# Kernel tuning notes

Measured on AMD Instinct MI355X. Metric: run time of the kernel, lower is better.

## Reference

```python
import jax, jax.numpy as jnp
import numpy as np

B, T, N = 32, 128, 30
D_T, D_V, D_I = 512, 512, 512


def setup_inputs() -> dict:
    key = jax.random.key(0)
    ks = jax.random.split(key, 9)
    return {
        "h_s": jax.random.normal(ks[0], (B, N, D_T), dtype=jnp.float32),
        "h_v": jax.random.normal(ks[1], (B, T, D_V), dtype=jnp.float32),
        "lengths": jax.random.randint(ks[2], (B,), 1, N + 1, dtype=jnp.int32),
        "W_S": jax.random.normal(ks[3], (D_T, D_I), dtype=jnp.float32) * 0.05,
        "b_S": jax.random.normal(ks[4], (D_I,), dtype=jnp.float32) * 0.05,
        "W_V": jax.random.normal(ks[5], (D_V, D_I), dtype=jnp.float32) * 0.05,
        "b_V": jax.random.normal(ks[6], (D_I,), dtype=jnp.float32) * 0.05,
        "W_w": jax.random.normal(ks[7], (D_I,), dtype=jnp.float32) * 0.05,
        "b_w": jax.random.normal(ks[8], (1,), dtype=jnp.float32) * 0.05,
    }


def reference(h_s, h_v, lengths, W_S, b_S, W_V, b_V, W_w, b_w):
    n_tok = h_s.shape[1]
    # token mask (B, N): 1 where position < length
    mask = (lengths[:, None] >= jnp.arange(1, n_tok + 1)[None, :]).astype(h_s.dtype)
    # loop-invariant projections computed once (the torch loop recomputes per t)
    S = h_s @ W_S + b_S                      # (B, N, D_I)
    V = h_v @ W_V + b_V                      # (B, T, D_I)
    # additive attention scores beta: (B, T, N)
    e = jnp.tanh(S[:, None, :, :] + V[:, :, None, :])  # (B, T, N, D_I)
    beta = jnp.einsum('btnd,d->btn', e, W_w) + b_w[0]
    # masked softmax (non-memory-efficient variant, faithful to source)
    m = mask[:, None, :]                      # (B, 1, N)
    p = jax.nn.softmax(beta * m, axis=-1) * m
    alpha = p / (p.sum(axis=-1, keepdims=True) + 1e-13) + 1e-13  # (B, T, N)
    # attended textual features: (B, T, D_T)
    return jnp.einsum('btn,bnd->btd', alpha, h_s)
```

## Files before the change

### kernel.cpp

```cpp
#include <hip/hip_runtime.h>
#include <math.h>

#define BB 32
#define TT 128
#define NTOK 30
#define DD 512
#define C2F 2.885390081777927f

typedef unsigned short u16;
typedef __attribute__((ext_vector_type(8))) short bf16x8;
typedef __attribute__((ext_vector_type(8))) unsigned short u16x8;
typedef __attribute__((ext_vector_type(4))) float f32x4;
typedef __attribute__((ext_vector_type(2))) _Float16 h16x2;

__device__ __forceinline__ u16 f2bf(float f) {
    unsigned u = __builtin_bit_cast(unsigned, f);
    u += 0x7fffu + ((u >> 16) & 1u);
    return (u16)(u >> 16);
}
__device__ __forceinline__ float bf2f(u16 u) {
    return __builtin_bit_cast(float, (unsigned)u << 16);
}
__device__ __forceinline__ u16 f2h(float f) {
    return __builtin_bit_cast(u16, (_Float16)f);
}

__device__ __forceinline__ void load_lds16(const u16* g, u16* l) {
    __builtin_amdgcn_global_load_lds(
        (const __attribute__((address_space(1))) unsigned int*)g,
        (__attribute__((address_space(3))) unsigned int*)l,
        16, 0, 0);
}

template<int CTRL>
__device__ __forceinline__ float dpp_add(float x) {
    int yi = __builtin_amdgcn_update_dpp(0, __builtin_bit_cast(int, x), CTRL, 0xF, 0xF, true);
    return x + __builtin_bit_cast(float, yi);
}
__device__ __forceinline__ float red64(float x) {
    x = dpp_add<0xB1>(x);
    x = dpp_add<0x4E>(x);
    x = dpp_add<0x141>(x);
    x = dpp_add<0x140>(x);
    x += __shfl_xor(x, 16, 64);
    x += __shfl_xor(x, 32, 64);
    return x;
}

#define NCONV ((BB*NTOK*DD + BB*TT*DD)/4/256)
__global__ __launch_bounds__(256) void prep(
    const float* __restrict__ h_s, const float* __restrict__ h_v,
    const float* __restrict__ W_S, const float* __restrict__ W_V,
    u16* __restrict__ Abf_s, u16* __restrict__ Abf_v,
    u16* __restrict__ WtS, u16* __restrict__ WtV)
{
    __shared__ u16 tile[32][33];
    int bx = blockIdx.x;
    if (bx < NCONV) {
        int i = bx * 256 + threadIdx.x;
        const int n0_4 = BB * NTOK * DD / 4;
        const float* x; u16* y;
        if (i < n0_4) { x = h_s; y = Abf_s; }
        else { i -= n0_4; x = h_v; y = Abf_v; }
        float4 v = ((const float4*)x)[i];
        ushort4 o;
        o.x = f2bf(v.x); o.y = f2bf(v.y); o.z = f2bf(v.z); o.w = f2bf(v.w);
        ((ushort4*)y)[i] = o;
        return;
    }
    int idx = bx - NCONV;
    const float* W = (idx & 256) ? W_V : W_S;
    u16*        T  = (idx & 256) ? WtV : WtS;
    idx &= 255;
    int k0 = (idx >> 4) * 32, n0 = (idx & 15) * 32;
    int c = threadIdx.x & 31, r8 = threadIdx.x >> 5;
    #pragma unroll
    for (int q = 0; q < 4; ++q) {
        int k = r8 + q * 8;
        tile[k][c] = f2bf(W[(size_t)(k0 + k) * DD + n0 + c]);
    }
    __syncthreads();
    #pragma unroll
    for (int q = 0; q < 4; ++q) {
        int n = r8 + q * 8;
        T[(size_t)(n0 + n) * DD + k0 + c] = tile[c][n];
    }
}

__global__ __launch_bounds__(256) void gemm_mfma(
    const u16* __restrict__ Abf_s, const u16* __restrict__ Abf_v,
    const u16* __restrict__ WtS, const u16* __restrict__ WtV,
    const float* __restrict__ b_S, const float* __restrict__ b_V,
    u16* __restrict__ Sh, u16* __restrict__ Vh)
{
    __shared__ u16 ldsA[64 * 64];
    __shared__ u16 ldsB[64 * 64];
    const int bid = blockIdx.x;
    const int grp = bid >> 6, rem = bid & 63;
    const int by  = rem >> 3;
    const int bxx = grp * 8 + (rem & 7);
    if (bxx >= 15 + 64) return;
    const u16* A; const u16* Bt; const float* bias; u16* Y; int bm;
    if (bxx < 15) { A = Abf_s; Bt = WtS; bias = b_S; Y = Sh; bm = bxx * 64; }
    else          { A = Abf_v; Bt = WtV; bias = b_V; Y = Vh; bm = (bxx - 15) * 64; }
    const int bn = by * 64;

    const int tid  = threadIdx.x;
    const int lane = tid & 63;
    const int wid  = tid >> 6;
    const int wr = wid >> 1, wc = wid & 1;

    const int idx0 = tid,       row0 = idx0 >> 3, ch0 = (idx0 & 7) ^ (row0 & 7);
    const int idx1 = 256 + tid, row1 = idx1 >> 3, ch1 = (idx1 & 7) ^ (row1 & 7);
    const u16* gA0 = A  + (size_t)(bm + row0) * DD + ch0 * 8;
    const u16* gA1 = A  + (size_t)(bm + row1) * DD + ch1 * 8;
    const u16* gB0 = Bt + (size_t)(bn + row0) * DD + ch0 * 8;
    const u16* gB1 = Bt + (size_t)(bn + row1) * DD + ch1 * 8;
    u16* lA0 = ldsA + wid * 512;
    u16* lA1 = ldsA + 2048 + wid * 512;
    u16* lB0 = ldsB + wid * 512;
    u16* lB1 = ldsB + 2048 + wid * 512;

    const int arow = wr * 32 + (lane & 15);
    const int brow = wc * 32 + (lane & 15);
    const int kq   = lane >> 4;
    const int sw   = lane & 7;

    f32x4 acc[2][2];
    #pragma unroll
    for (int i = 0; i < 2; ++i)
        #pragma unroll
        for (int j = 0; j < 2; ++j)
            acc[i][j] = (f32x4){0.f, 0.f, 0.f, 0.f};

    for (int k0 = 0; k0 < DD; k0 += 64) {
        __syncthreads();
        load_lds16(gA0 + k0, lA0);
        load_lds16(gA1 + k0, lA1);
        load_lds16(gB0 + k0, lB0);
        load_lds16(gB1 + k0, lB1);
        __syncthreads();

        bf16x8 af[2][2], bfr[2][2];
        #pragma unroll
        for (int i = 0; i < 2; ++i)
            #pragma unroll
            for (int s = 0; s < 2; ++s) {
                int ra = arow + i * 16;
                af[i][s]  = *(const bf16x8*)(ldsA + ra * 64 + ((s * 4 + kq) ^ sw) * 8);
                int rb = brow + i * 16;
                bfr[i][s] = *(const bf16x8*)(ldsB + rb * 64 + ((s * 4 + kq) ^ sw) * 8);
            }
        #pragma unroll
        for (int s = 0; s < 2; ++s)
            #pragma unroll
            for (int i = 0; i < 2; ++i)
                #pragma unroll
                for (int j = 0; j < 2; ++j)
                    acc[i][j] = __builtin_amdgcn_mfma_f32_16x16x32_bf16(
                        af[i][s], bfr[j][s], acc[i][j], 0, 0, 0);
    }

    #pragma unroll
    for (int i = 0; i < 2; ++i)
        #pragma unroll
        for (int j = 0; j < 2; ++j) {
            int r = bm + wr * 32 + i * 16 + (lane >> 4) * 4;
            int c = bn + wc * 32 + j * 16 + (lane & 15);
            float bv = bias[c];
            #pragma unroll
            for (int reg = 0; reg < 4; ++reg)
                Y[(size_t)(r + reg) * DD + c] = f2h((acc[i][j][reg] + bv) * C2F);
        }
}

__global__ __launch_bounds__(512) void attend5(
    const u16* __restrict__ Sh, const u16* __restrict__ Vh,
    const u16* __restrict__ Hbf, const int* __restrict__ lengths,
    const float* __restrict__ W_w, const float* __restrict__ b_w,
    float* __restrict__ out)
{
    __shared__ u16 Sl[NTOK * DD];
    __shared__ u16 Hl[NTOK * DD];
    const int b  = blockIdx.x >> 4;
    const int tc = blockIdx.x & 15;
    const int tid  = threadIdx.x;
    const int w    = tid >> 6;
    const int lane = tid & 63;
    const int t_glob = tc * 8 + w;
    const int len = lengths[b];
    const int d0 = lane * 8;
    const float bwv = b_w[0];

    {
        const uint4* sS = (const uint4*)(Sh + (size_t)b * NTOK * DD);
        const uint4* sH = (const uint4*)(Hbf + (size_t)b * NTOK * DD);
        uint4* dS = (uint4*)Sl;
        uint4* dH = (uint4*)Hl;
        #pragma unroll
        for (int i = 0; i < 4; ++i) {
            int idx = i * 512 + tid;
            if (idx < NTOK * DD / 8) { dS[idx] = sS[idx]; dH[idx] = sH[idx]; }
        }
    }

    h16x2 vv[4], w2[4];
    float wsum;
    {
        u16x8 v8 = *(const u16x8*)(Vh + ((size_t)(b * TT + t_glob)) * DD + d0);
        float4 w0 = *(const float4*)&W_w[d0];
        float4 w1 = *(const float4*)&W_w[d0 + 4];
        float wwf[8] = {w0.x, w0.y, w0.z, w0.w, w1.x, w1.y, w1.z, w1.w};
        #pragma unroll
        for (int p = 0; p < 4; ++p) {
            vv[p] = __builtin_bit_cast(h16x2, ((const unsigned int*)&v8)[p]);
            w2[p] = (h16x2){(_Float16)wwf[2 * p], (_Float16)wwf[2 * p + 1]};
        }
        float wpart = 0.f;
        #pragma unroll
        for (int j = 0; j < 8; ++j) wpart += wwf[j];
        wsum = red64(wpart);
    }

    __syncthreads();

    const h16x2 one2 = (h16x2){(_Float16)1.0f, (_Float16)1.0f};
    float pacc[NTOK];
    #pragma unroll
    for (int n = 0; n < NTOK; ++n) {
        u16x8 s8 = *(const u16x8*)(Sl + n * DD + d0);
        float a = 0.f;
        #pragma unroll
        for (int p = 0; p < 4; ++p) {
            h16x2 s2 = __builtin_bit_cast(h16x2, ((const unsigned int*)&s8)[p]);
            h16x2 t = s2 + vv[p];
            h16x2 e;
            e.x = __builtin_elementwise_exp2(t.x);
            e.y = __builtin_elementwise_exp2(t.y);
            h16x2 f = e + one2;
            h16x2 r;
            r.x = __builtin_amdgcn_rcph(f.x);
            r.y = __builtin_amdgcn_rcph(f.y);
            a = __builtin_amdgcn_fdot2(r, w2[p], a, false);
        }
        pacc[n] = red64(a);
    }

    float mx = -1e30f;
    #pragma unroll
    for (int n = 0; n < NTOK; ++n) {
        float bn = fmaf(-2.f, pacc[n], wsum + bwv);
        pacc[n] = bn;
        if (n < len) mx = fmaxf(mx, bn);
    }
    float ssum = 0.f;
    #pragma unroll
    for (int n = 0; n < NTOK; ++n) {
        float e = (n < len) ? __expf(pacc[n] - mx) : 0.f;
        pacc[n] = e;
        ssum += e;
    }
    const float inv = 1.f / (ssum + 1e-13f);
    #pragma unroll
    for (int n = 0; n < NTOK; ++n) pacc[n] = fmaf(pacc[n], inv, 1e-13f);

    float acc8[8] = {};
    #pragma unroll
    for (int n = 0; n < NTOK; ++n) {
        float a = pacc[n];
        u16x8 h8 = *(const u16x8*)(Hl + n * DD + d0);
        #pragma unroll
        for (int j = 0; j < 8; ++j)
            acc8[j] = fmaf(a, bf2f(h8[j]), acc8[j]);
    }
    float* Or = out + ((size_t)(b * TT + t_glob)) * DD + d0;
    *(float4*)&Or[0] = make_float4(acc8[0], acc8[1], acc8[2], acc8[3]);
    *(float4*)&Or[4] = make_float4(acc8[4], acc8[5], acc8[6], acc8[7]);
}

extern "C" void kernel_launch(void* const* d_in, const int* in_sizes, int n_in,
                              void* d_out, int out_size, void* d_ws, size_t ws_size,
                              hipStream_t stream) {
    const float* h_s     = (const float*)d_in[0];
    const float* h_v     = (const float*)d_in[1];
    const int*   lengths = (const int*)  d_in[2];
    const float* W_S     = (const float*)d_in[3];
    const float* b_S     = (const float*)d_in[4];
    const float* W_V     = (const float*)d_in[5];
    const float* b_V     = (const float*)d_in[6];
    const float* W_w     = (const float*)d_in[7];
    const float* b_w     = (const float*)d_in[8];
    float* out = (float*)d_out;

    u16* Sh    = (u16*)d_ws;
    u16* Vh    = Sh + (size_t)BB * NTOK * DD;
    u16* WtS   = Vh + (size_t)BB * TT * DD;
    u16* WtV   = WtS + (size_t)DD * DD;
    u16* Abf_s = WtV + (size_t)DD * DD;
    u16* Abf_v = Abf_s + (size_t)BB * NTOK * DD;

    prep<<<NCONV + 512, 256, 0, stream>>>(h_s, h_v, W_S, W_V, Abf_s, Abf_v, WtS, WtV);
    gemm_mfma<<<640, 256, 0, stream>>>(
        Abf_s, Abf_v, WtS, WtV, b_S, b_V, Sh, Vh);
    attend5<<<BB * 16, 512, 0, stream>>>(Sh, Vh, Abf_s, lengths, W_w, b_w, out);
}
```

Before: 42.39 us.

## Read S and H directly from global in attention kernel, use fp32 math

The attention kernel no longer stages the per-batch S and H tiles in LDS. Each wave instead reads rows straight from global memory (relying on L2 reuse), and blocks shrink to 256 threads with batch-interleaved block indexing. The tanh-sigmoid evaluation moves from packed fp16 to fp32 exp2/rcp with scalar FMAs. This removes the LDS fill and the barrier and frees occupancy, at the cost of more global traffic and roughly twice the transcendental instructions.

Result: no change. 41.58 us, median of 2 (-1.9%).

```diff
diff --git a/kernel.cpp b/kernel.cpp
--- a/kernel.cpp
+++ b/kernel.cpp
@@ -11,7 +11,6 @@
 typedef __attribute__((ext_vector_type(8))) short bf16x8;
 typedef __attribute__((ext_vector_type(8))) unsigned short u16x8;
 typedef __attribute__((ext_vector_type(4))) float f32x4;
-typedef __attribute__((ext_vector_type(2))) _Float16 h16x2;
 
 __device__ __forceinline__ u16 f2bf(float f) {
     unsigned u = __builtin_bit_cast(unsigned, f);
@@ -23,6 +22,9 @@
 }
 __device__ __forceinline__ u16 f2h(float f) {
     return __builtin_bit_cast(u16, (_Float16)f);
+}
+__device__ __forceinline__ float h2f(u16 u) {
+    return (float)__builtin_bit_cast(_Float16, u);
 }
 
 __device__ __forceinline__ void load_lds16(const u16* g, u16* l) {
@@ -174,74 +176,49 @@
         }
 }
 
-__global__ __launch_bounds__(512) void attend5(
+__global__ __launch_bounds__(256) void attend6(
     const u16* __restrict__ Sh, const u16* __restrict__ Vh,
     const u16* __restrict__ Hbf, const int* __restrict__ lengths,
     const float* __restrict__ W_w, const float* __restrict__ b_w,
     float* __restrict__ out)
 {
-    __shared__ u16 Sl[NTOK * DD];
-    __shared__ u16 Hl[NTOK * DD];
-    const int b  = blockIdx.x >> 4;
-    const int tc = blockIdx.x & 15;
-    const int tid  = threadIdx.x;
-    const int w    = tid >> 6;
-    const int lane = tid & 63;
-    const int t_glob = tc * 8 + w;
-    const int len = lengths[b];
-    const int d0 = lane * 8;
+    const int bid  = blockIdx.x;
+    const int b    = bid & 31;
+    const int tq   = bid >> 5;
+    const int wv   = threadIdx.x >> 6;
+    const int lane = threadIdx.x & 63;
+    const int t    = tq * 4 + wv;
+    const int len  = lengths[b];
+    const int d0   = lane * 8;
     const float bwv = b_w[0];
 
+    const u16* Srow = Sh  + (size_t)b * NTOK * DD + d0;
+    const u16* Hrow = Hbf + (size_t)b * NTOK * DD + d0;
+
+    float v[8], ww[8];
     {
-        const uint4* sS = (const uint4*)(Sh + (size_t)b * NTOK * DD);
-        const uint4* sH = (const uint4*)(Hbf + (size_t)b * NTOK * DD);
-        uint4* dS = (uint4*)Sl;
-        uint4* dH = (uint4*)Hl;
-        #pragma unroll
-        for (int i = 0; i < 4; ++i) {
-            int idx = i * 512 + tid;
-            if (idx < NTOK * DD / 8) { dS[idx] = sS[idx]; dH[idx] = sH[idx]; }
-        }
-    }
-
-    h16x2 vv[4], w2[4];
-    float wsum;
-    {
-        u16x8 v8 = *(const u16x8*)(Vh + ((size_t)(b * TT + t_glob)) * DD + d0);
+        u16x8 v8 = *(const u16x8*)(Vh + ((size_t)(b * TT + t)) * DD + d0);
         float4 w0 = *(const float4*)&W_w[d0];
         float4 w1 = *(const float4*)&W_w[d0 + 4];
-        float wwf[8] = {w0.x, w0.y, w0.z, w0.w, w1.x, w1.y, w1.z, w1.w};
-        #pragma unroll
-        for (int p = 0; p < 4; ++p) {
-            vv[p] = __builtin_bit_cast(h16x2, ((const unsigned int*)&v8)[p]);
-            w2[p] = (h16x2){(_Float16)wwf[2 * p], (_Float16)wwf[2 * p + 1]};
-        }
-        float wpart = 0.f;
-        #pragma unroll
-        for (int j = 0; j < 8; ++j) wpart += wwf[j];
-        wsum = red64(wpart);
-    }
-
-    __syncthreads();
-
-    const h16x2 one2 = (h16x2){(_Float16)1.0f, (_Float16)1.0f};
+        #pragma unroll
+        for (int j = 0; j < 8; ++j) v[j] = h2f(v8[j]);
+        ww[0]=w0.x; ww[1]=w0.y; ww[2]=w0.z; ww[3]=w0.w;
+        ww[4]=w1.x; ww[5]=w1.y; ww[6]=w1.z; ww[7]=w1.w;
+    }
+    float wpart = 0.f;
+    #pragma unroll
+    for (int j = 0; j < 8; ++j) wpart += ww[j];
+    const float wsum = red64(wpart);
+
     float pacc[NTOK];
     #pragma unroll
     for (int n = 0; n < NTOK; ++n) {
-        u16x8 s8 = *(const u16x8*)(Sl + n * DD + d0);
+        u16x8 s8 = *(const u16x8*)(Srow + (size_t)n * DD);
         float a = 0.f;
         #pragma unroll
-        for (int p = 0; p < 4; ++p) {
-            h16x2 s2 = __builtin_bit_cast(h16x2, ((const unsigned int*)&s8)[p]);
-            h16x2 t = s2 + vv[p];
-            h16x2 e;
-            e.x = __builtin_elementwise_exp2(t.x);
-            e.y = __builtin_elementwise_exp2(t.y);
-            h16x2 f = e + one2;
-            h16x2 r;
-            r.x = __builtin_amdgcn_rcph(f.x);
-            r.y = __builtin_amdgcn_rcph(f.y);
-            a = __builtin_amdgcn_fdot2(r, w2[p], a, false);
+        for (int j = 0; j < 8; ++j) {
+            float e = __builtin_amdgcn_exp2f(h2f(s8[j]) + v[j]);
+            a = fmaf(ww[j], __builtin_amdgcn_rcpf(1.f + e), a);
         }
         pacc[n] = red64(a);
     }
@@ -268,12 +245,12 @@
     #pragma unroll
     for (int n = 0; n < NTOK; ++n) {
         float a = pacc[n];
-        u16x8 h8 = *(const u16x8*)(Hl + n * DD + d0);
+        u16x8 h8 = *(const u16x8*)(Hrow + (size_t)n * DD);
         #pragma unroll
         for (int j = 0; j < 8; ++j)
             acc8[j] = fmaf(a, bf2f(h8[j]), acc8[j]);
     }
-    float* Or = out + ((size_t)(b * TT + t_glob)) * DD + d0;
+    float* Or = out + ((size_t)(b * TT + t)) * DD + d0;
     *(float4*)&Or[0] = make_float4(acc8[0], acc8[1], acc8[2], acc8[3]);
     *(float4*)&Or[4] = make_float4(acc8[4], acc8[5], acc8[6], acc8[7]);
 }
@@ -302,5 +279,5 @@
     prep<<<NCONV + 512, 256, 0, stream>>>(h_s, h_v, W_S, W_V, Abf_s, Abf_v, WtS, WtV);
     gemm_mfma<<<640, 256, 0, stream>>>(
         Abf_s, Abf_v, WtS, WtV, b_S, b_V, Sh, Vh);
-    attend5<<<BB * 16, 512, 0, stream>>>(Sh, Vh, Abf_s, lengths, W_w, b_w, out);
-}
+    attend6<<<1024, 256, 0, stream>>>(Sh, Vh, Abf_s, lengths, W_w, b_w, out);
+}
```
